# Performance work log

Hardware: AMD Instinct MI355X
Metric: run time of the kernel (lower is better)

The kernel has to match this reference:

```python
import jax, jax.numpy as jnp
import numpy as np

D_MODEL = 512
NH_ATTN = 8
D_STATE = 64
HEADDIM = 128
D_INNER = 2 * D_MODEL          # 1024
NHEADS = D_INNER // HEADDIM    # 8
CONV_K = 4
CONV_DIM = D_INNER + 2 * D_STATE            # 1152
D_IN_PROJ = 2 * D_INNER + 2 * D_STATE + NHEADS  # 2184
B, S, M = 2, 2048, 1024
EPS = 1e-5


def setup_inputs() -> dict:
    key = jax.random.key(0)
    ks = jax.random.split(key, 10)
    s = 0.02
    return {
        'x': jax.random.normal(ks[0], (B, S, D_MODEL), dtype=jnp.float32),
        'memory': jax.random.normal(ks[1], (B, M, D_MODEL), dtype=jnp.float32),
        'pad_mask': jnp.ones((B, S, 1), dtype=jnp.float32),
        'ln1_g': jnp.ones((D_MODEL,)), 'ln1_b': jnp.zeros((D_MODEL,)),
        'ln2_g': jnp.ones((D_MODEL,)), 'ln2_b': jnp.zeros((D_MODEL,)),
        'W_in': jax.random.normal(ks[2], (D_IN_PROJ, D_MODEL)) * s,
        'conv_w': jax.random.normal(ks[3], (CONV_DIM, 1, CONV_K)) * s,
        'conv_b': jnp.zeros((CONV_DIM,)),
        'dt_bias': jnp.log(jnp.expm1(jax.random.uniform(ks[4], (NHEADS,), minval=0.001, maxval=0.1))),
        'A_log': jnp.log(jnp.arange(1, NHEADS + 1, dtype=jnp.float32)),
        'D_skip': jnp.ones((NHEADS,)),
        'rms_w': jnp.ones((D_INNER,)),
        'W_out': jax.random.normal(ks[5], (D_MODEL, D_INNER)) * s,
        'Wqkv': jax.random.normal(ks[6], (3 * D_MODEL, D_MODEL)) * s,
        'bqkv': jnp.zeros((3 * D_MODEL,)),
        'Wo': jax.random.normal(ks[7], (D_MODEL, D_MODEL)) * s,
        'bo': jnp.zeros((D_MODEL,)),
    }


def _layernorm(x, g, b):
    m = jnp.mean(x, axis=-1, keepdims=True)
    v = jnp.mean((x - m) ** 2, axis=-1, keepdims=True)
    return (x - m) * jax.lax.rsqrt(v + EPS) * g + b


def _mamba(x, W_in, conv_w, conv_b, dt_bias, A_log, D_skip, rms_w, W_out):
    b, s, _ = x.shape
    zxbcdt = x @ W_in.T                                     # [b,s,2184]
    z, xBC, dt = jnp.split(zxbcdt, [D_INNER, D_INNER + CONV_DIM], axis=-1)
    # causal depthwise conv over time on (x, B, C)
    xt = jnp.transpose(xBC, (0, 2, 1))                      # [b,C,s]
    xt = jax.lax.conv_general_dilated(
        xt, conv_w, (1,), [(CONV_K - 1, 0)],
        feature_group_count=CONV_DIM,
        dimension_numbers=('NCH', 'OIH', 'NCH'))
    xBC = jax.nn.silu(jnp.transpose(xt, (0, 2, 1)) + conv_b)
    xs, Bm, Cm = jnp.split(xBC, [D_INNER, D_INNER + D_STATE], axis=-1)
    dt = jax.nn.softplus(dt + dt_bias)                      # [b,s,H]
    A = -jnp.exp(A_log)                                     # [H]
    xh = xs.reshape(b, s, NHEADS, HEADDIM)                  # [b,s,H,P]

    def step(h, inps):
        dt_t, B_t, C_t, x_t = inps                          # [b,H],[b,N],[b,N],[b,H,P]
        decay = jnp.exp(dt_t * A)                           # [b,H]
        h = h * decay[..., None, None] + (dt_t[..., None, None] * x_t[..., None]) * B_t[:, None, None, :]
        y = jnp.einsum('bhpn,bn->bhp', h, C_t)
        return h, y

    h0 = jnp.zeros((b, NHEADS, HEADDIM, D_STATE), dtype=x.dtype)
    _, ys = jax.lax.scan(step, h0, (dt.transpose(1, 0, 2), Bm.transpose(1, 0, 2),
                                    Cm.transpose(1, 0, 2), xh.transpose(1, 0, 2, 3)))
    y = ys.transpose(1, 0, 2, 3) + D_skip[None, None, :, None] * xh
    y = y.reshape(b, s, D_INNER) * jax.nn.silu(z)           # gated
    y = y * jax.lax.rsqrt(jnp.mean(y * y, axis=-1, keepdims=True) + EPS) * rms_w
    return y @ W_out.T


def _cross_attn(q_in, memory, Wqkv, bqkv, Wo, bo):
    b, s, _ = q_in.shape
    m = memory.shape[1]
    dh = D_MODEL // NH_ATTN
    q = (q_in @ Wqkv[:D_MODEL].T + bqkv[:D_MODEL]).reshape(b, s, NH_ATTN, dh)
    k = (memory @ Wqkv[D_MODEL:2 * D_MODEL].T + bqkv[D_MODEL:2 * D_MODEL]).reshape(b, m, NH_ATTN, dh)
    v = (memory @ Wqkv[2 * D_MODEL:].T + bqkv[2 * D_MODEL:]).reshape(b, m, NH_ATTN, dh)
    scores = jnp.einsum('bqhd,bkhd->bhqk', q, k) / jnp.sqrt(jnp.asarray(dh, q.dtype))
    p = jax.nn.softmax(scores, axis=-1)
    out = jnp.einsum('bhqk,bkhd->bqhd', p, v).reshape(b, s, D_MODEL)
    return out @ Wo.T + bo


def reference(x, memory, pad_mask, ln1_g, ln1_b, ln2_g, ln2_b, W_in, conv_w, conv_b,
              dt_bias, A_log, D_skip, rms_w, W_out, Wqkv, bqkv, Wo, bo):
    residual = x
    xn = _layernorm(x, ln1_g, ln1_b) * pad_mask
    x = residual + _mamba(xn, W_in, conv_w, conv_b, dt_bias, A_log, D_skip, rms_w, W_out)
    h = _layernorm(x, ln2_g, ln2_b)
    x = x + _cross_attn(h, memory, Wqkv, bqkv, Wo, bo)
    return x
```

## Files before the change

kernel.cpp:

```cpp
#include <hip/hip_runtime.h>
#include <hip/hip_bf16.h>

typedef __hip_bfloat16 bf16;
typedef short v8s __attribute__((ext_vector_type(8)));
typedef short v4s __attribute__((ext_vector_type(4)));
typedef float v4f __attribute__((ext_vector_type(4)));

__device__ __forceinline__ void gll16(const bf16* g, bf16* l) {
    __builtin_amdgcn_global_load_lds(
        (const __attribute__((address_space(1))) unsigned int*)g,
        (__attribute__((address_space(3))) unsigned int*)l, 16, 0, 0);
}
__device__ __forceinline__ float bf2f(short s) {
    return __uint_as_float(((unsigned int)(unsigned short)s) << 16);
}
__device__ __forceinline__ short f2bfs(float f) {
    return (short)__bfloat16_as_ushort(__float2bfloat16(f));
}

__global__ __launch_bounds__(256) void pre_kernel(
    const float* __restrict__ x, const float* __restrict__ g,
    const float* __restrict__ bt, const float* __restrict__ mask,
    bf16* __restrict__ xn,
    const float* __restrict__ W_in, const float* __restrict__ W_out,
    const float* __restrict__ Wqkv, const float* __restrict__ Wo,
    const float* __restrict__ mem,
    bf16* __restrict__ Winb, bf16* __restrict__ Woutb, bf16* __restrict__ Wqkvb,
    bf16* __restrict__ Wob, bf16* __restrict__ memb)
{
    int tid = threadIdx.x;
    if (blockIdx.x < 4096) {
        int row = blockIdx.x;
        const float* xr = x + (size_t)row * 512;
        float v0 = xr[tid], v1 = xr[tid + 256];
        float s = v0 + v1, ss = v0 * v0 + v1 * v1;
        #pragma unroll
        for (int o = 32; o; o >>= 1) { s += __shfl_xor(s, o); ss += __shfl_xor(ss, o); }
        __shared__ float l1[4], l2[4];
        if ((tid & 63) == 0) { l1[tid >> 6] = s; l2[tid >> 6] = ss; }
        __syncthreads();
        s = l1[0] + l1[1] + l1[2] + l1[3];
        ss = l2[0] + l2[1] + l2[2] + l2[3];
        float mean = s * (1.f / 512.f);
        float var = ss * (1.f / 512.f) - mean * mean;
        float rs = rsqrtf(var + 1e-5f);
        float mk = mask[row];
        xn[(size_t)row * 512 + tid] =
            __float2bfloat16(((v0 - mean) * rs * g[tid] + bt[tid]) * mk);
        xn[(size_t)row * 512 + tid + 256] =
            __float2bfloat16(((v1 - mean) * rs * g[tid + 256] + bt[tid + 256]) * mk);
        return;
    }
    int i = (blockIdx.x - 4096) * 256 + tid;
    const int E0 = 2184 * 512;
    const int E1 = E0 + 524288;
    const int E2 = E1 + 786432;
    const int E3 = E2 + 262144;
    const int E4 = E3 + 1048576;
    if (i < E0) {
        Winb[i] = __float2bfloat16(W_in[i]);
    } else if (i < E1) {
        int j = i - E0; Woutb[j] = __float2bfloat16(W_out[j]);
    } else if (i < E2) {
        int j = i - E1; Wqkvb[j] = __float2bfloat16(Wqkv[j]);
    } else if (i < E3) {
        int j = i - E2; Wob[j] = __float2bfloat16(Wo[j]);
    } else if (i < E4) {
        int j = i - E3; memb[j] = __float2bfloat16(mem[j]);
    }
}

__global__ __launch_bounds__(256) void ln_kernel(
    const float* __restrict__ x, const float* __restrict__ g,
    const float* __restrict__ bt, bf16* __restrict__ out)
{
    int row = blockIdx.x, tid = threadIdx.x;
    const float* xr = x + (size_t)row * 512;
    float v0 = xr[tid], v1 = xr[tid + 256];
    float s = v0 + v1, ss = v0 * v0 + v1 * v1;
    #pragma unroll
    for (int o = 32; o; o >>= 1) { s += __shfl_xor(s, o); ss += __shfl_xor(ss, o); }
    __shared__ float l1[4], l2[4];
    if ((tid & 63) == 0) { l1[tid >> 6] = s; l2[tid >> 6] = ss; }
    __syncthreads();
    s = l1[0] + l1[1] + l1[2] + l1[3];
    ss = l2[0] + l2[1] + l2[2] + l2[3];
    float mean = s * (1.f / 512.f);
    float var = ss * (1.f / 512.f) - mean * mean;
    float rs = rsqrtf(var + 1e-5f);
    out[(size_t)row * 512 + tid] =
        __float2bfloat16((v0 - mean) * rs * g[tid] + bt[tid]);
    out[(size_t)row * 512 + tid + 256] =
        __float2bfloat16((v1 - mean) * rs * g[tid + 256] + bt[tid + 256]);
}

__global__ __launch_bounds__(256) void gemm_bt(
    const bf16* __restrict__ Aall, const bf16* __restrict__ Wall,
    const float* __restrict__ bias, const float* __restrict__ resid,
    void* __restrict__ Cout,
    int M, int N, int K, int ldA, int ldW, int ldC,
    long sA1, long sA2, long sW1, long sW2, long sC1, long sC2,
    int zdiv, int outbf16)
{
    __shared__ bf16 lA[2][128 * 32];
    __shared__ bf16 lB[2][128 * 32];
    int z = blockIdx.z;
    int zb = z / zdiv, zh = z - zb * zdiv;
    const bf16* A = Aall + zb * sA1 + zh * sA2;
    const bf16* W = Wall + zb * sW1 + zh * sW2;
    long coff = zb * sC1 + zh * sC2;

    int bm = blockIdx.x * 128, bn = blockIdx.y * 128;
    int tid = threadIdx.x, lane = tid & 63, wv = tid >> 6;
    int wr = (wv >> 1) * 64, wc = (wv & 1) * 64;
    int lr15 = lane & 15, lk8 = (lane >> 4) * 8;

    v4f acc[4][4] = {};
    int sr = tid >> 2, sc = (tid & 3) * 8;
    const bf16* Abase = A + (size_t)(bm + sr) * ldA + sc;
    const bf16* Wbase = W + (size_t)(bn + sr) * ldW + sc;

    int nt = K >> 5, cur = 0;
    gll16(Abase, &lA[0][tid * 8]);
    gll16(Abase + (size_t)64 * ldA, &lA[0][tid * 8 + 2048]);
    gll16(Wbase, &lB[0][tid * 8]);
    gll16(Wbase + (size_t)64 * ldW, &lB[0][tid * 8 + 2048]);
    __syncthreads();
    for (int t = 0; t < nt; ++t) {
        if (t + 1 < nt) {
            int k0 = (t + 1) * 32;
            gll16(Abase + k0, &lA[cur ^ 1][tid * 8]);
            gll16(Abase + (size_t)64 * ldA + k0, &lA[cur ^ 1][tid * 8 + 2048]);
            gll16(Wbase + k0, &lB[cur ^ 1][tid * 8]);
            gll16(Wbase + (size_t)64 * ldW + k0, &lB[cur ^ 1][tid * 8 + 2048]);
        }
        v8s af[4], bfr[4];
        #pragma unroll
        for (int i = 0; i < 4; ++i)
            af[i] = *(const v8s*)&lA[cur][(wr + i * 16 + lr15) * 32 + lk8];
        #pragma unroll
        for (int i = 0; i < 4; ++i)
            bfr[i] = *(const v8s*)&lB[cur][(wc + i * 16 + lr15) * 32 + lk8];
        #pragma unroll
        for (int mi = 0; mi < 4; ++mi)
            #pragma unroll
            for (int ni = 0; ni < 4; ++ni)
                acc[mi][ni] = __builtin_amdgcn_mfma_f32_16x16x32_bf16(
                    af[mi], bfr[ni], acc[mi][ni], 0, 0, 0);
        __syncthreads();
        cur ^= 1;
    }
    int r0 = bm + wr + (lane >> 4) * 4;
    int c0 = bn + wc + lr15;
    #pragma unroll
    for (int mi = 0; mi < 4; ++mi) {
        #pragma unroll
        for (int ni = 0; ni < 4; ++ni) {
            int col = c0 + ni * 16;
            if (col < N) {
                float bv = bias ? bias[col] : 0.f;
                #pragma unroll
                for (int r = 0; r < 4; ++r) {
                    int row = r0 + mi * 16 + r;
                    long idx = coff + (long)row * ldC + col;
                    float v = acc[mi][ni][r] + bv;
                    if (resid) v += resid[idx];
                    if (outbf16) ((bf16*)Cout)[idx] = __float2bfloat16(v);
                    else ((float*)Cout)[idx] = v;
                }
            }
        }
    }
}

__global__ __launch_bounds__(256) void gemm64(
    const bf16* __restrict__ Aall, const bf16* __restrict__ Wall,
    const float* __restrict__ bias, const float* __restrict__ resid,
    void* __restrict__ Cout,
    int M, int N, int K, int ldA, int ldW, int ldC,
    long sA1, long sA2, long sW1, long sW2, long sC1, long sC2,
    int zdiv, int outbf16, bf16* __restrict__ vTout)
{
    __shared__ bf16 lA[2][64 * 32];
    __shared__ bf16 lB[2][64 * 32];
    int z = blockIdx.z;
    int zb = z / zdiv, zh = z - zb * zdiv;
    const bf16* A = Aall + zb * sA1 + zh * sA2;
    const bf16* W = Wall + zb * sW1 + zh * sW2;
    long coff = zb * sC1 + zh * sC2;

    int bm = blockIdx.x * 64, bn = blockIdx.y * 64;
    int tid = threadIdx.x, lane = tid & 63, wv = tid >> 6;
    int wr = (wv >> 1) * 32, wc = (wv & 1) * 32;
    int lr15 = lane & 15, lk8 = (lane >> 4) * 8;

    v4f acc[2][2] = {};
    int sr = tid >> 2, sc = (tid & 3) * 8;
    const bf16* Abase = A + (size_t)(bm + sr) * ldA + sc;
    const bf16* Wbase = W + (size_t)(bn + sr) * ldW + sc;

    int nt = K >> 5, cur = 0;
    gll16(Abase, &lA[0][tid * 8]);
    gll16(Wbase, &lB[0][tid * 8]);
    __syncthreads();
    for (int t = 0; t < nt; ++t) {
        if (t + 1 < nt) {
            int k0 = (t + 1) * 32;
            gll16(Abase + k0, &lA[cur ^ 1][tid * 8]);
            gll16(Wbase + k0, &lB[cur ^ 1][tid * 8]);
        }
        v8s a0 = *(const v8s*)&lA[cur][(wr + lr15) * 32 + lk8];
        v8s a1 = *(const v8s*)&lA[cur][(wr + 16 + lr15) * 32 + lk8];
        v8s b0 = *(const v8s*)&lB[cur][(wc + lr15) * 32 + lk8];
        v8s b1 = *(const v8s*)&lB[cur][(wc + 16 + lr15) * 32 + lk8];
        acc[0][0] = __builtin_amdgcn_mfma_f32_16x16x32_bf16(a0, b0, acc[0][0], 0, 0, 0);
        acc[0][1] = __builtin_amdgcn_mfma_f32_16x16x32_bf16(a0, b1, acc[0][1], 0, 0, 0);
        acc[1][0] = __builtin_amdgcn_mfma_f32_16x16x32_bf16(a1, b0, acc[1][0], 0, 0, 0);
        acc[1][1] = __builtin_amdgcn_mfma_f32_16x16x32_bf16(a1, b1, acc[1][1], 0, 0, 0);
        __syncthreads();
        cur ^= 1;
    }
    int r0 = bm + wr + (lane >> 4) * 4;
    int c0 = bn + wc + lr15;
    #pragma unroll
    for (int mi = 0; mi < 2; ++mi) {
        #pragma unroll
        for (int ni = 0; ni < 2; ++ni) {
            int col = c0 + ni * 16;
            if (col < N) {
                float bv = bias ? bias[col] : 0.f;
                float vals[4];
                #pragma unroll
                for (int r = 0; r < 4; ++r) {
                    int row = r0 + mi * 16 + r;
                    long idx = coff + (long)row * ldC + col;
                    float v = acc[mi][ni][r] + bv;
                    if (resid) v += resid[idx];
                    vals[r] = v;
                    if (outbf16) ((bf16*)Cout)[idx] = __float2bfloat16(v);
                    else ((float*)Cout)[idx] = v;
                }
                if (vTout && col >= 512) {
                    int d = col - 512;
                    int row0 = r0 + mi * 16;
                    int bb = row0 >> 10, m0 = row0 & 1023;
                    v4s pk;
                    #pragma unroll
                    for (int r = 0; r < 4; ++r) pk[r] = f2bfs(vals[r]);
                    *(v4s*)(vTout + (((size_t)(bb * 8 + (d >> 6)) * 64 + (d & 63))
                                     * 1024 + m0)) = pk;
                }
            }
        }
    }
}

__global__ __launch_bounds__(256) void flash_attn(
    const bf16* __restrict__ qb, const bf16* __restrict__ kvb,
    const bf16* __restrict__ vT, bf16* __restrict__ attn)
{
    __shared__ bf16 lK[2][128 * 64];
    __shared__ bf16 lV[2][64 * 128];
    __shared__ bf16 lP[4][16 * 128];
    int z = blockIdx.z;
    int b = z >> 3, h = z & 7;
    int q0 = blockIdx.x * 64;
    int tid = threadIdx.x, lane = tid & 63, wv = tid >> 6;
    int l15 = lane & 15, l4 = lane >> 4, l7 = lane & 7;

    const bf16* Qg = qb + (size_t)(b * 2048 + q0) * 512 + h * 64;
    const bf16* Kg = kvb + (size_t)b * 1024 * 1024 + h * 64;
    const bf16* Vg = vT + (size_t)z * 64 * 1024;

    v8s af[2];
    #pragma unroll
    for (int ks = 0; ks < 2; ++ks)
        af[ks] = *(const v8s*)(Qg + (size_t)(wv * 16 + l15) * 512 + (ks * 4 + l4) * 8);

    #pragma unroll
    for (int pass = 0; pass < 4; ++pass) {
        int s = pass * 256 + tid;
        int kr = s >> 3, kc = s & 7;
        gll16(Kg + (size_t)kr * 1024 + ((kc ^ (kr & 7)) << 3), &lK[0][s * 8]);
        int vr = s >> 4, vc = s & 15;
        int vsw = (vc & 8) | ((vc & 7) ^ (vr & 7));
        gll16(Vg + (size_t)vr * 1024 + (vsw << 3), &lV[0][s * 8]);
    }
    __syncthreads();

    v4f o[4] = {};
    v4f m_run = (v4f){-1e30f, -1e30f, -1e30f, -1e30f};
    v4f l_run = (v4f){0.f, 0.f, 0.f, 0.f};
    bf16* lPw = &lP[wv][0];

    int cur = 0;
    #pragma unroll 1
    for (int t = 0; t < 8; ++t) {
        if (t + 1 < 8) {
            int k0n = (t + 1) * 128;
            #pragma unroll
            for (int pass = 0; pass < 4; ++pass) {
                int s = pass * 256 + tid;
                int kr = s >> 3, kc = s & 7;
                gll16(Kg + (size_t)(k0n + kr) * 1024 + ((kc ^ (kr & 7)) << 3),
                      &lK[cur ^ 1][s * 8]);
                int vr = s >> 4, vc = s & 15;
                int vsw = (vc & 8) | ((vc & 7) ^ (vr & 7));
                gll16(Vg + (size_t)vr * 1024 + k0n + (vsw << 3), &lV[cur ^ 1][s * 8]);
            }
        }
        v4f s_acc[8];
        #pragma unroll
        for (int kn = 0; kn < 8; ++kn) {
            s_acc[kn] = (v4f){0.f, 0.f, 0.f, 0.f};
            #pragma unroll
            for (int ks = 0; ks < 2; ++ks) {
                v8s kv = *(const v8s*)&lK[cur][(kn * 16 + l15) * 64 +
                                               (((ks * 4 + l4) ^ l7) << 3)];
                s_acc[kn] = __builtin_amdgcn_mfma_f32_16x16x32_bf16(
                    af[ks], kv, s_acc[kn], 0, 0, 0);
            }
        }
        v4f tm;
        #pragma unroll
        for (int r = 0; r < 4; ++r) {
            float m0 = fmaxf(fmaxf(s_acc[0][r], s_acc[1][r]),
                             fmaxf(s_acc[2][r], s_acc[3][r]));
            float m1 = fmaxf(fmaxf(s_acc[4][r], s_acc[5][r]),
                             fmaxf(s_acc[6][r], s_acc[7][r]));
            tm[r] = fmaxf(m0, m1);
        }
        #pragma unroll
        for (int off = 8; off >= 1; off >>= 1)
            #pragma unroll
            for (int r = 0; r < 4; ++r)
                tm[r] = fmaxf(tm[r], __shfl_xor(tm[r], off));
        v4f mnew, alpha;
        #pragma unroll
        for (int r = 0; r < 4; ++r) {
            mnew[r] = fmaxf(m_run[r], 0.125f * tm[r]);
            alpha[r] = __expf(m_run[r] - mnew[r]);
        }
        m_run = mnew;
        v4f rs = {0.f, 0.f, 0.f, 0.f};
        #pragma unroll
        for (int kn = 0; kn < 8; ++kn)
            #pragma unroll
            for (int r = 0; r < 4; ++r) {
                float pv = __expf(0.125f * s_acc[kn][r] - mnew[r]);
                s_acc[kn][r] = pv;
                rs[r] += pv;
            }
        #pragma unroll
        for (int off = 8; off >= 1; off >>= 1)
            #pragma unroll
            for (int r = 0; r < 4; ++r)
                rs[r] += __shfl_xor(rs[r], off);
        #pragma unroll
        for (int r = 0; r < 4; ++r)
            l_run[r] = l_run[r] * alpha[r] + rs[r];
        #pragma unroll
        for (int ni = 0; ni < 4; ++ni)
            #pragma unroll
            for (int r = 0; r < 4; ++r)
                o[ni][r] *= alpha[r];
        #pragma unroll
        for (int kn = 0; kn < 8; ++kn)
            #pragma unroll
            for (int r = 0; r < 4; ++r) {
                int row = l4 * 4 + r;
                int col = kn * 16 + l15;
                int c = col >> 3;
                int csw = (c & 8) | ((c & 7) ^ (row & 7));
                lPw[row * 128 + (csw << 3) + (col & 7)] =
                    __float2bfloat16(s_acc[kn][r]);
            }
        #pragma unroll
        for (int ni = 0; ni < 4; ++ni)
            #pragma unroll
            for (int ks = 0; ks < 4; ++ks) {
                int ck = ks * 4 + l4;
                int psw = (ck & 8) | ((ck & 7) ^ l7);
                v8s pv = *(const v8s*)&lPw[l15 * 128 + (psw << 3)];
                v8s vv = *(const v8s*)&lV[cur][(ni * 16 + l15) * 128 + (psw << 3)];
                o[ni] = __builtin_amdgcn_mfma_f32_16x16x32_bf16(
                    pv, vv, o[ni], 0, 0, 0);
            }
        __syncthreads();
        cur ^= 1;
    }
    v4f inv;
    #pragma unroll
    for (int r = 0; r < 4; ++r) inv[r] = 1.f / l_run[r];
    #pragma unroll
    for (int ni = 0; ni < 4; ++ni)
        #pragma unroll
        for (int r = 0; r < 4; ++r) {
            int row = q0 + wv * 16 + l4 * 4 + r;
            int col = h * 64 + ni * 16 + l15;
            attn[(size_t)(b * 2048 + row) * 512 + col] =
                __float2bfloat16(o[ni][r] * inv[r]);
        }
}

__global__ __launch_bounds__(256) void conv_dt(
    const bf16* __restrict__ zx, const float* __restrict__ cw,
    const float* __restrict__ cb, bf16* __restrict__ out,
    const float* __restrict__ dt_bias, const float* __restrict__ A_log,
    float* __restrict__ dtb, float* __restrict__ decb)
{
    int tid = threadIdx.x;
    if (blockIdx.x >= 576) {
        int i = (blockIdx.x - 576) * 256 + tid;
        if (i >= 32768) return;
        int h = i & 7, row = i >> 3;
        float d = bf2f(((const short*)zx)[(size_t)row * 2184 + 2176 + h]) + dt_bias[h];
        float sp = d > 20.f ? d : log1pf(expf(d));
        dtb[i] = sp;
        decb[i] = expf(-expf(A_log[h]) * sp);
        return;
    }
    int idx = blockIdx.x * 256 + tid;
    int c4 = (idx % 288) * 4;
    int tb = (idx / 288) % 256;
    int b  = idx / (288 * 256);
    int t0 = tb * 8;
    const bf16* base = zx + (size_t)b * 2048 * 2184 + 1024 + c4;
    bf16* ob = out + ((size_t)(b * 2048 + t0)) * 1152 + c4;

    float wt[4][4];
    #pragma unroll
    for (int k = 0; k < 4; ++k)
        #pragma unroll
        for (int j = 0; j < 4; ++j) wt[j][k] = cw[(c4 + k) * 4 + j];
    v4f bias = *(const v4f*)(cb + c4);

    v4f r[11];
    #pragma unroll
    for (int j = 0; j < 11; ++j) {
        int ts = t0 - 3 + j;
        if (ts >= 0) {
            v4s raw = *(const v4s*)(base + (size_t)ts * 2184);
            #pragma unroll
            for (int k = 0; k < 4; ++k) r[j][k] = bf2f(raw[k]);
        } else r[j] = (v4f){0.f, 0.f, 0.f, 0.f};
    }
    #pragma unroll
    for (int t = 0; t < 8; ++t) {
        v4f acc = bias;
        #pragma unroll
        for (int k = 0; k < 4; ++k)
            acc[k] += wt[0][k] * r[t][k] + wt[1][k] * r[t + 1][k]
                    + wt[2][k] * r[t + 2][k] + wt[3][k] * r[t + 3][k];
        v4s res;
        #pragma unroll
        for (int k = 0; k < 4; ++k) {
            float v = acc[k] / (1.f + expf(-acc[k]));
            res[k] = f2bfs(v);
        }
        *(v4s*)(ob + (size_t)t * 1152) = res;
    }
}

__global__ __launch_bounds__(256) void scan_p1(
    const bf16* __restrict__ conv, const float* __restrict__ dtb,
    const float* __restrict__ decb, const float* __restrict__ A_log,
    bf16* __restrict__ slocal, float* __restrict__ cdec)
{
    int chunk = blockIdx.x, bh = blockIdx.y;
    int b = bh >> 3, h = bh & 7;
    int tid = threadIdx.x;
    int wv = tid >> 6, lane = tid & 63;
    int nh = lane >> 5, psub = lane & 31;
    int p = wv * 32 + psub;
    __shared__ float lx[32][128];
    __shared__ float lB[32][64];
    __shared__ float ldt[32], ldec[32];
    const bf16* cb_ = conv + (size_t)b * 2048 * 1152;
    int t0 = chunk * 32;
    #pragma unroll
    for (int pass = 0; pass < 2; ++pass) {
        int s = pass * 256 + tid;
        int row = s >> 4, c8 = (s & 15) * 8;
        v8s raw = *(const v8s*)(cb_ + (size_t)(t0 + row) * 1152 + h * 128 + c8);
        v4f lo, hi;
        #pragma unroll
        for (int j = 0; j < 4; ++j) { lo[j] = bf2f(raw[j]); hi[j] = bf2f(raw[j + 4]); }
        *(v4f*)&lx[row][c8] = lo;
        *(v4f*)&lx[row][c8 + 4] = hi;
    }
    {
        int s = tid;
        int row = s >> 3, c8 = (s & 7) * 8;
        v8s raw = *(const v8s*)(cb_ + (size_t)(t0 + row) * 1152 + 1024 + c8);
        v4f lo, hi;
        #pragma unroll
        for (int j = 0; j < 4; ++j) { lo[j] = bf2f(raw[j]); hi[j] = bf2f(raw[j + 4]); }
        *(v4f*)&lB[row][c8] = lo;
        *(v4f*)&lB[row][c8 + 4] = hi;
    }
    if (tid < 32) {
        int ri = (b * 2048 + t0 + tid) * 8 + h;
        ldt[tid] = dtb[ri]; ldec[tid] = decb[ri];
    }
    __syncthreads();
    v4f hs[8] = {};
    float sdt = 0.f;
    #pragma unroll 2
    for (int t = 0; t < 32; ++t) {
        float dtv = ldt[t], dec = ldec[t];
        float c1 = dtv * lx[t][p];
        const v4f* Bp = (const v4f*)&lB[t][nh * 32];
        #pragma unroll
        for (int i = 0; i < 8; ++i) hs[i] = hs[i] * dec + Bp[i] * c1;
        sdt += dtv;
    }
    if (tid == 0) cdec[bh * 64 + chunk] = expf(-expf(A_log[h]) * sdt);
    bf16* S = slocal + ((size_t)bh * 64 + chunk) * 8192;
    #pragma unroll
    for (int i = 0; i < 8; ++i)
        #pragma unroll
        for (int j = 0; j < 4; ++j)
            S[(nh * 32 + i * 4 + j) * 128 + p] = __float2bfloat16(hs[i][j]);
}

__global__ __launch_bounds__(256) void scan_comb(
    const bf16* __restrict__ slocal, const float* __restrict__ cdec,
    bf16* __restrict__ hinit)
{
    int e = blockIdx.x * 256 + threadIdx.x;
    int bh = e >> 13, np = e & 8191;
    size_t base = (size_t)bh * 524288 + np;
    const float* cd = cdec + bh * 64;
    float hi = 0.f;
    for (int c = 0; c < 64; ++c) {
        size_t idx = base + (size_t)c * 8192;
        hinit[idx] = __float2bfloat16(hi);
        hi = hi * cd[c] + __bfloat162float(slocal[idx]);
    }
}

__global__ __launch_bounds__(256) void scan_p3(
    const bf16* __restrict__ conv, const float* __restrict__ dtb,
    const float* __restrict__ decb, const bf16* __restrict__ hinit,
    const float* __restrict__ Dskip, bf16* __restrict__ ybuf)
{
    int chunk = blockIdx.x, bh = blockIdx.y;
    int b = bh >> 3, h = bh & 7;
    int tid = threadIdx.x;
    int wv = tid >> 6, lane = tid & 63;
    int nh = lane >> 5, psub = lane & 31;
    int p = wv * 32 + psub;
    __shared__ float lx[32][128];
    __shared__ float lB[32][64];
    __shared__ float lC[32][64];
    __shared__ float ldt[32], ldec[32];
    const bf16* cb_ = conv + (size_t)b * 2048 * 1152;
    int t0 = chunk * 32;
    #pragma unroll
    for (int pass = 0; pass < 2; ++pass) {
        int s = pass * 256 + tid;
        int row = s >> 4, c8 = (s & 15) * 8;
        v8s raw = *(const v8s*)(cb_ + (size_t)(t0 + row) * 1152 + h * 128 + c8);
        v4f lo, hi;
        #pragma unroll
        for (int j = 0; j < 4; ++j) { lo[j] = bf2f(raw[j]); hi[j] = bf2f(raw[j + 4]); }
        *(v4f*)&lx[row][c8] = lo;
        *(v4f*)&lx[row][c8 + 4] = hi;
    }
    {
        int s = tid;
        int row = s >> 3, c8 = (s & 7) * 8;
        v8s rawB = *(const v8s*)(cb_ + (size_t)(t0 + row) * 1152 + 1024 + c8);
        v8s rawC = *(const v8s*)(cb_ + (size_t)(t0 + row) * 1152 + 1088 + c8);
        v4f lo, hi;
        #pragma unroll
        for (int j = 0; j < 4; ++j) { lo[j] = bf2f(rawB[j]); hi[j] = bf2f(rawB[j + 4]); }
        *(v4f*)&lB[row][c8] = lo;
        *(v4f*)&lB[row][c8 + 4] = hi;
        #pragma unroll
        for (int j = 0; j < 4; ++j) { lo[j] = bf2f(rawC[j]); hi[j] = bf2f(rawC[j + 4]); }
        *(v4f*)&lC[row][c8] = lo;
        *(v4f*)&lC[row][c8 + 4] = hi;
    }
    if (tid < 32) {
        int ri = (b * 2048 + t0 + tid) * 8 + h;
        ldt[tid] = dtb[ri]; ldec[tid] = decb[ri];
    }
    __syncthreads();
    v4f hs[8];
    const bf16* H = hinit + ((size_t)bh * 64 + chunk) * 8192;
    #pragma unroll
    for (int i = 0; i < 8; ++i)
        #pragma unroll
        for (int j = 0; j < 4; ++j)
            hs[i][j] = __bfloat162float(H[(nh * 32 + i * 4 + j) * 128 + p]);
    float Dk = Dskip[h];
    #pragma unroll 2
    for (int t = 0; t < 32; ++t) {
        float dtv = ldt[t], dec = ldec[t];
        float xv = lx[t][p];
        float c1 = dtv * xv;
        const v4f* Bp = (const v4f*)&lB[t][nh * 32];
        const v4f* Cp = (const v4f*)&lC[t][nh * 32];
        v4f ya = {0.f, 0.f, 0.f, 0.f};
        #pragma unroll
        for (int i = 0; i < 8; ++i) {
            hs[i] = hs[i] * dec + Bp[i] * c1;
            ya += hs[i] * Cp[i];
        }
        float part = ya[0] + ya[1] + ya[2] + ya[3];
        part += __shfl_xor(part, 32);
        if (nh == 0)
            ybuf[((size_t)(b * 2048 + t0 + t)) * 1024 + h * 128 + p] =
                __float2bfloat16(part + Dk * xv);
    }
}

__global__ __launch_bounds__(256) void gate_rms(
    const bf16* __restrict__ ybuf, const bf16* __restrict__ zx,
    const float* __restrict__ rms_w, bf16* __restrict__ out)
{
    int row = blockIdx.x, tid = threadIdx.x;
    int i0 = tid * 4;
    v4s yv = *(const v4s*)(ybuf + (size_t)row * 1024 + i0);
    v4s zv = *(const v4s*)(zx + (size_t)row * 2184 + i0);
    v4f rw = *(const v4f*)(rms_w + i0);
    float vals[4];
    float ss = 0.f;
    #pragma unroll
    for (int j = 0; j < 4; ++j) {
        float y = bf2f(yv[j]);
        float z = bf2f(zv[j]);
        float g = y * (z / (1.f + expf(-z)));
        vals[j] = g;
        ss += g * g;
    }
    #pragma unroll
    for (int o = 32; o; o >>= 1) ss += __shfl_xor(ss, o);
    __shared__ float l[4];
    if ((tid & 63) == 0) l[tid >> 6] = ss;
    __syncthreads();
    ss = l[0] + l[1] + l[2] + l[3];
    float rs = rsqrtf(ss * (1.f / 1024.f) + 1e-5f);
    v4s o4;
    #pragma unroll
    for (int j = 0; j < 4; ++j)
        o4[j] = f2bfs(vals[j] * rs * rw[j]);
    *(v4s*)(out + (size_t)row * 1024 + i0) = o4;
}

extern "C" void kernel_launch(void* const* d_in, const int* in_sizes, int n_in,
                              void* d_out, int out_size, void* d_ws, size_t ws_size,
                              hipStream_t stream) {
    (void)in_sizes; (void)n_in; (void)out_size; (void)ws_size;
    const float* x       = (const float*)d_in[0];
    const float* memory  = (const float*)d_in[1];
    const float* mask    = (const float*)d_in[2];
    const float* ln1_g   = (const float*)d_in[3];
    const float* ln1_b   = (const float*)d_in[4];
    const float* ln2_g   = (const float*)d_in[5];
    const float* ln2_b   = (const float*)d_in[6];
    const float* W_in    = (const float*)d_in[7];
    const float* conv_w  = (const float*)d_in[8];
    const float* conv_b  = (const float*)d_in[9];
    const float* dt_bias = (const float*)d_in[10];
    const float* A_log   = (const float*)d_in[11];
    const float* D_skip  = (const float*)d_in[12];
    const float* rms_w   = (const float*)d_in[13];
    const float* W_out   = (const float*)d_in[14];
    const float* Wqkv    = (const float*)d_in[15];
    const float* bqkv    = (const float*)d_in[16];
    const float* Wo      = (const float*)d_in[17];
    const float* bo      = (const float*)d_in[18];
    float* out = (float*)d_out;

    char* w = (char*)d_ws;
    bf16*  xn     = (bf16*)(w + 0);
    bf16*  Winb   = (bf16*)(w + 4194304);
    bf16*  Woutb  = (bf16*)(w + 6430720);
    bf16*  Wqkvb  = (bf16*)(w + 7479296);
    bf16*  Wob    = (bf16*)(w + 9052160);
    bf16*  memb   = (bf16*)(w + 9576448);
    bf16*  zx     = (bf16*)(w + 11673600);
    bf16*  gout   = (bf16*)(w + 29564928);
    bf16*  conv   = (bf16*)(w + 47456256);
    float* dtb    = (float*)(w + 66330624);
    float* decb   = (float*)(w + 66461696);
    bf16*  ybuf   = (bf16*)(w + 66592768);
    bf16*  slocal = (bf16*)(w + 83369984);
    bf16*  hinit  = (bf16*)(w + 100147200);
    float* x2     = (float*)(w + 100147200);
    bf16*  hb     = (bf16*)(w + 108535808);
    bf16*  qb     = (bf16*)(w + 112730112);
    float* cdec   = (float*)(w + 116924416);
    bf16*  kvb    = (bf16*)(w + 116928512);
    bf16*  vT     = (bf16*)(w + 121122816);
    bf16*  attn   = (bf16*)(w + 123219968);

    pre_kernel<<<18704, 256, 0, stream>>>(x, ln1_g, ln1_b, mask, xn,
                                          W_in, W_out, Wqkv, Wo, memory,
                                          Winb, Woutb, Wqkvb, Wob, memb);

    gemm_bt<<<dim3(32, 18, 1), 256, 0, stream>>>(
        xn, Winb, nullptr, nullptr, (void*)zx,
        4096, 2184, 512, 512, 512, 2184,
        0, 0, 0, 0, 0, 0, 1, 1);

    conv_dt<<<704, 256, 0, stream>>>(zx, conv_w, conv_b, conv,
                                     dt_bias, A_log, dtb, decb);

    scan_p1<<<dim3(64, 16), 256, 0, stream>>>(conv, dtb, decb, A_log, slocal, cdec);
    scan_comb<<<512, 256, 0, stream>>>(slocal, cdec, hinit);
    scan_p3<<<dim3(64, 16), 256, 0, stream>>>(conv, dtb, decb, hinit, D_skip, ybuf);

    gate_rms<<<4096, 256, 0, stream>>>(ybuf, zx, rms_w, gout);

    gemm64<<<dim3(64, 8, 1), 256, 0, stream>>>(
        gout, Woutb, nullptr, x, (void*)x2,
        4096, 512, 1024, 1024, 1024, 512,
        0, 0, 0, 0, 0, 0, 1, 0, nullptr);

    ln_kernel<<<4096, 256, 0, stream>>>(x2, ln2_g, ln2_b, hb);

    gemm64<<<dim3(64, 8, 1), 256, 0, stream>>>(
        hb, Wqkvb, bqkv, nullptr, (void*)qb,
        4096, 512, 512, 512, 512, 512, 0, 0, 0, 0, 0, 0, 1, 1, nullptr);
    gemm64<<<dim3(32, 16, 1), 256, 0, stream>>>(
        memb, Wqkvb + 512 * 512, bqkv + 512, nullptr, (void*)kvb,
        2048, 1024, 512, 512, 512, 1024, 0, 0, 0, 0, 0, 0, 1, 1, vT);

    flash_attn<<<dim3(32, 1, 16), 256, 0, stream>>>(qb, kvb, vT, attn);

    gemm64<<<dim3(64, 8, 1), 256, 0, stream>>>(
        attn, Wob, bo, x2, (void*)out,
        4096, 512, 512, 512, 512, 512,
        0, 0, 0, 0, 0, 0, 1, 0, nullptr);
}
```

Before: 194.0 us.

## Swizzle workgroups across XCDs, raise MFMA priority, vectorize scan combine

Remaps workgroup IDs in the GEMM and flash-attention kernels so neighbouring tiles land on the same XCD, which is meant to improve L2 reuse of shared A/W and K/V tiles. It also brackets the MFMA sections of flash attention with s_setprio so matrix work is favoured over other waves. The scan_comb kernel now handles two state elements per thread with 32-bit packed loads and stores, halving its grid. The GEMM swizzle assumes the workgroup count divides evenly by 8, and a remainder could leave some tiles unmapped.

```diff
diff --git a/kernel.cpp b/kernel.cpp
--- a/kernel.cpp
+++ b/kernel.cpp
@@ -94,6 +94,16 @@
         __float2bfloat16((v1 - mean) * rs * g[tid + 256] + bt[tid + 256]);
 }
 
+__device__ __forceinline__ void xcd_swz(int& bx, int& by) {
+    int gx = gridDim.x;
+    int nwg = gx * gridDim.y;
+    int wg = bx + gx * by;
+    int cpx = nwg >> 3;
+    int nw = (wg & 7) * cpx + (wg >> 3);
+    bx = nw % gx;
+    by = nw / gx;
+}
+
 __global__ __launch_bounds__(256) void gemm_bt(
     const bf16* __restrict__ Aall, const bf16* __restrict__ Wall,
     const float* __restrict__ bias, const float* __restrict__ resid,
@@ -110,7 +120,9 @@
     const bf16* W = Wall + zb * sW1 + zh * sW2;
     long coff = zb * sC1 + zh * sC2;
 
-    int bm = blockIdx.x * 128, bn = blockIdx.y * 128;
+    int bxs = blockIdx.x, bys = blockIdx.y;
+    xcd_swz(bxs, bys);
+    int bm = bxs * 128, bn = bys * 128;
     int tid = threadIdx.x, lane = tid & 63, wv = tid >> 6;
     int wr = (wv >> 1) * 64, wc = (wv & 1) * 64;
     int lr15 = lane & 15, lk8 = (lane >> 4) * 8;
@@ -189,7 +201,9 @@
     const bf16* W = Wall + zb * sW1 + zh * sW2;
     long coff = zb * sC1 + zh * sC2;
 
-    int bm = blockIdx.x * 64, bn = blockIdx.y * 64;
+    int bxs = blockIdx.x, bys = blockIdx.y;
+    xcd_swz(bxs, bys);
+    int bm = bxs * 64, bn = bys * 64;
     int tid = threadIdx.x, lane = tid & 63, wv = tid >> 6;
     int wr = (wv >> 1) * 32, wc = (wv & 1) * 32;
     int lr15 = lane & 15, lk8 = (lane >> 4) * 8;
@@ -262,9 +276,11 @@
     __shared__ bf16 lK[2][128 * 64];
     __shared__ bf16 lV[2][64 * 128];
     __shared__ bf16 lP[4][16 * 128];
-    int z = blockIdx.z;
+    int wg = blockIdx.x + 32 * blockIdx.z;
+    int nw = (wg & 7) * 64 + (wg >> 3);
+    int z = nw >> 5;
     int b = z >> 3, h = z & 7;
-    int q0 = blockIdx.x * 64;
+    int q0 = (nw & 31) * 64;
     int tid = threadIdx.x, lane = tid & 63, wv = tid >> 6;
     int l15 = lane & 15, l4 = lane >> 4, l7 = lane & 7;
 
@@ -310,6 +326,7 @@
             }
         }
         v4f s_acc[8];
+        __builtin_amdgcn_s_setprio(1);
         #pragma unroll
         for (int kn = 0; kn < 8; ++kn) {
             s_acc[kn] = (v4f){0.f, 0.f, 0.f, 0.f};
@@ -321,6 +338,7 @@
                     af[ks], kv, s_acc[kn], 0, 0, 0);
             }
         }
+        __builtin_amdgcn_s_setprio(0);
         v4f tm;
         #pragma unroll
         for (int r = 0; r < 4; ++r) {
@@ -375,6 +393,7 @@
                 lPw[row * 128 + (csw << 3) + (col & 7)] =
                     __float2bfloat16(s_acc[kn][r]);
             }
+        __builtin_amdgcn_s_setprio(1);
         #pragma unroll
         for (int ni = 0; ni < 4; ++ni)
             #pragma unroll
@@ -386,6 +405,7 @@
                 o[ni] = __builtin_amdgcn_mfma_f32_16x16x32_bf16(
                     pv, vv, o[ni], 0, 0, 0);
             }
+        __builtin_amdgcn_s_setprio(0);
         __syncthreads();
         cur ^= 1;
     }
@@ -529,14 +549,19 @@
     bf16* __restrict__ hinit)
 {
     int e = blockIdx.x * 256 + threadIdx.x;
-    int bh = e >> 13, np = e & 8191;
-    size_t base = (size_t)bh * 524288 + np;
+    int bh = e >> 12, np2 = e & 4095;
+    size_t base = (size_t)bh * 524288 + (size_t)np2 * 2;
     const float* cd = cdec + bh * 64;
-    float hi = 0.f;
+    float h0 = 0.f, h1 = 0.f;
     for (int c = 0; c < 64; ++c) {
         size_t idx = base + (size_t)c * 8192;
-        hinit[idx] = __float2bfloat16(hi);
-        hi = hi * cd[c] + __bfloat162float(slocal[idx]);
+        unsigned int raw = *(const unsigned int*)(slocal + idx);
+        unsigned int pk = (unsigned int)(unsigned short)f2bfs(h0) |
+                          ((unsigned int)(unsigned short)f2bfs(h1) << 16);
+        *(unsigned int*)(hinit + idx) = pk;
+        float cdv = cd[c];
+        h0 = h0 * cdv + bf2f((short)(raw & 0xffff));
+        h1 = h1 * cdv + bf2f((short)(raw >> 16));
     }
 }
 
@@ -711,7 +736,7 @@
                                      dt_bias, A_log, dtb, decb);
 
     scan_p1<<<dim3(64, 16), 256, 0, stream>>>(conv, dtb, decb, A_log, slocal, cdec);
-    scan_comb<<<512, 256, 0, stream>>>(slocal, cdec, hinit);
+    scan_comb<<<256, 256, 0, stream>>>(slocal, cdec, hinit);
     scan_p3<<<dim3(64, 16), 256, 0, stream>>>(conv, dtb, decb, hinit, D_skip, ybuf);
 
     gate_rms<<<4096, 256, 0, stream>>>(ybuf, zx, rms_w, gout);
```

Result: slower. 198.8 us (+2.5%).
